# Kernel optimization log

Hardware: AMD Instinct MI355X
Metric: run time of the kernel (lower is better)

## Reference

```python
import jax, jax.numpy as jnp
import numpy as np

TEMPERATURE = 0.07
EPS = 1e-12


def setup_inputs() -> dict:
    key = jax.random.key(0)
    k1, k2 = jax.random.split(key)
    N, D = 8192, 1024
    features = jax.random.normal(k1, (N, D), dtype=jnp.float32)
    labels = jax.random.randint(k2, (N,), 0, 1000, dtype=jnp.int64)
    return {"features": features, "labels": labels}


def reference(features, labels):
    # L2-normalize rows (matches F.normalize(dim=1) with its eps clamp)
    norm = jnp.maximum(jnp.linalg.norm(features, axis=1, keepdims=True), 1e-12)
    f = features / norm
    n = f.shape[0]
    # [N, N] similarity
    sim = jnp.matmul(f, f.T) / TEMPERATURE
    # positive-pair mask from labels
    mask = (labels[:, None] == labels[None, :]).astype(sim.dtype)
    # denominator excludes self-similarity via (1 - eye)
    not_self = 1.0 - jnp.eye(n, dtype=sim.dtype)
    exp_sim = jnp.exp(sim) * not_self
    log_prob = sim - jnp.log(exp_sim.sum(axis=1, keepdims=True) + EPS)
    loss = -(mask * log_prob).sum(axis=1) / (mask.sum(axis=1) + EPS)
    return loss.mean()
```

## Files before the change

kernel.cpp:

```cpp
#include <hip/hip_runtime.h>
#include <hip/hip_bf16.h>

#define N_ROWS 8192
#define DIM 1024
#define TEMP_INV (1.0f / 0.07f)
#define LOG2E 1.4426950408889634f
#define LN2 0.6931471805599453f

typedef __attribute__((ext_vector_type(4))) int i32x4;

__device__ inline void gload_lds16(const void* g, void* l) {
    __builtin_amdgcn_global_load_lds(
        (const __attribute__((address_space(1))) void*)g,
        (__attribute__((address_space(3))) void*)l,
        16, 0, 0);
}

__global__ __launch_bounds__(256) void knorm(const float* __restrict__ X,
                                             char* __restrict__ Q,
                                             float* __restrict__ SC,
                                             float* __restrict__ S1,
                                             float* __restrict__ S2,
                                             float* __restrict__ CNT) {
    const int row = blockIdx.x;
    const int t = threadIdx.x;
    const float* x = X + (size_t)row * DIM;
    float4 v = reinterpret_cast<const float4*>(x)[t];
    float ss = v.x * v.x + v.y * v.y + v.z * v.z + v.w * v.w;
    float mx = fmaxf(fmaxf(fabsf(v.x), fabsf(v.y)), fmaxf(fabsf(v.z), fabsf(v.w)));
    #pragma unroll
    for (int off = 32; off > 0; off >>= 1) {
        ss += __shfl_down(ss, off);
        mx = fmaxf(mx, __shfl_down(mx, off));
    }
    __shared__ float redS[4], redM[4];
    if ((t & 63) == 0) { redS[t >> 6] = ss; redM[t >> 6] = mx; }
    __syncthreads();
    float tot = redS[0] + redS[1] + redS[2] + redS[3];
    float amax = fmaxf(fmaxf(redM[0], redM[1]), fmaxf(redM[2], redM[3]));
    amax = fmaxf(amax, 1e-20f);
    const float norm = fmaxf(sqrtf(tot), 1e-12f);
    const float qmul = 127.0f / amax;
    const float scale = amax / (127.0f * norm);
    int q0 = (int)rintf(v.x * qmul);
    int q1 = (int)rintf(v.y * qmul);
    int q2 = (int)rintf(v.z * qmul);
    int q3 = (int)rintf(v.w * qmul);
    q0 = min(max(q0, -127), 127); q1 = min(max(q1, -127), 127);
    q2 = min(max(q2, -127), 127); q3 = min(max(q3, -127), 127);
    const unsigned packed = (unsigned)(q0 & 0xff) | ((unsigned)(q1 & 0xff) << 8) |
                            ((unsigned)(q2 & 0xff) << 16) | ((unsigned)(q3 & 0xff) << 24);
    reinterpret_cast<unsigned*>(Q + (size_t)row * DIM)[t] = packed;
    if (t == 0) SC[row] = scale;
    if (t == 1) { S1[row] = 0.f; S2[row] = 0.f; CNT[row] = 0.f; }
}

__global__ __launch_bounds__(256) void kgemm(const char* __restrict__ Q,
                                             const float* __restrict__ SC,
                                             const int* __restrict__ labels,
                                             float* __restrict__ S1,
                                             float* __restrict__ S2,
                                             float* __restrict__ CNT) {
    constexpr int BM = 128, BK = 128;
    __shared__ __align__(16) char As[BM * BK];
    __shared__ __align__(16) char Bs[BM * BK];
    __shared__ int labR[BM];
    __shared__ int labC[BM];
    __shared__ float scR[BM];
    __shared__ float scCs[BM];

    const int bid0 = blockIdx.x;
    const int bid = (bid0 & 7) * 260 + (bid0 >> 3);
    int a = (int)((sqrtf(8.0f * (float)bid + 1.0f) - 1.0f) * 0.5f);
    while ((a + 1) * (a + 2) / 2 <= bid) ++a;
    while (a * (a + 1) / 2 > bid) --a;
    const int bx = a;
    const int by = bid - a * (a + 1) / 2;
    const bool diag = (bx == by);
    const int rowBase = by * BM;
    const int colBase = bx * BM;

    const int t = threadIdx.x;
    const int lane = t & 63;
    const int wid = t >> 6;
    const int wr = wid >> 1;
    const int wc = wid & 1;
    const int l16 = lane & 15;
    const int g16 = lane >> 4;

    if (t < 128) { labR[t] = labels[rowBase + t]; scR[t] = SC[rowBase + t]; }
    else {
        labC[t - 128] = labels[colBase + (t - 128)];
        scCs[t - 128] = SC[colBase + (t - 128)] * (TEMP_INV * LOG2E);
    }

    i32x4 acc[4][4];
    #pragma unroll
    for (int m = 0; m < 4; ++m)
        #pragma unroll
        for (int n = 0; n < 4; ++n)
            acc[m][n] = i32x4{0, 0, 0, 0};

    const int srow = t >> 3;
    const int scolL = (t & 7) * 16;
    const int xorb = (l16 & 7) << 4;

    const char* srcA[4];
    const char* srcB[4];
    int dstOff[4];
    #pragma unroll
    for (int i = 0; i < 4; ++i) {
        const int r = i * 32 + srow;
        const int sg = scolL ^ ((r & 7) << 4);
        srcA[i] = Q + (size_t)(rowBase + r) * DIM + sg;
        srcB[i] = Q + (size_t)(colBase + r) * DIM + sg;
        dstOff[i] = r * BK + scolL;
    }

    #pragma unroll
    for (int kt = 0; kt < DIM / BK; ++kt) {
        const int k0 = kt * BK;
        #pragma unroll
        for (int i = 0; i < 4; ++i) {
            gload_lds16(srcA[i] + k0, &As[dstOff[i]]);
            gload_lds16(srcB[i] + k0, &Bs[dstOff[i]]);
        }
        __syncthreads();

        #pragma unroll
        for (int kk = 0; kk < 2; ++kk) {
            const int ck = (kk * 64 + g16 * 16) ^ xorb;
            i32x4 av[4], bv[4];
            #pragma unroll
            for (int m = 0; m < 4; ++m)
                av[m] = *reinterpret_cast<const i32x4*>(&As[(wr * 64 + m * 16 + l16) * BK + ck]);
            #pragma unroll
            for (int n = 0; n < 4; ++n)
                bv[n] = *reinterpret_cast<const i32x4*>(&Bs[(wc * 64 + n * 16 + l16) * BK + ck]);
            #pragma unroll
            for (int m = 0; m < 4; ++m)
                #pragma unroll
                for (int n = 0; n < 4; ++n)
                    acc[m][n] = __builtin_amdgcn_mfma_i32_16x16x64_i8(av[m], bv[n], acc[m][n], 0, 0, 0);
        }
        __syncthreads();
    }

    int labCn[4];
    float scCl2[4];
    #pragma unroll
    for (int n = 0; n < 4; ++n) {
        const int c = wc * 64 + n * 16 + l16;
        labCn[n] = labC[c];
        scCl2[n] = scCs[c];
    }

    const unsigned long long grpmask = 0xFFFFull << (g16 * 16);

    float colE[4]  = {0.f, 0.f, 0.f, 0.f};
    float colS2[4] = {0.f, 0.f, 0.f, 0.f};
    float colC[4]  = {0.f, 0.f, 0.f, 0.f};

    #pragma unroll
    for (int m = 0; m < 4; ++m) {
        const int rloc = wr * 64 + m * 16 + g16 * 4;
        #pragma unroll
        for (int reg = 0; reg < 4; ++reg) {
            const int row = rowBase + rloc + reg;
            const int labRow = labR[rloc + reg];
            const float sRow = scR[rloc + reg];
            float e = 0.f, s2 = 0.f, c = 0.f;
            #pragma unroll
            for (int n = 0; n < 4; ++n) {
                const float arg2 = (float)acc[m][n][reg] * sRow * scCl2[n];
                const int col = colBase + wc * 64 + n * 16 + l16;
                const float ex = __builtin_amdgcn_exp2f(arg2);
                const bool same = (labRow == labCn[n]);
                if (diag) {
                    if (row != col) e += ex;
                } else {
                    e += ex;
                    colE[n] += ex;
                }
                if (same) {
                    const float sim = arg2 * LN2;
                    s2 += sim; c += 1.0f;
                    if (!diag) { colS2[n] += sim; colC[n] += 1.0f; }
                }
            }
            const unsigned long long bal = __ballot(c != 0.f);
            const bool doS = (bal & grpmask) != 0ull;
            #pragma unroll
            for (int off = 1; off < 16; off <<= 1) e += __shfl_xor(e, off);
            if (doS) {
                #pragma unroll
                for (int off = 1; off < 16; off <<= 1) {
                    s2 += __shfl_xor(s2, off);
                    c  += __shfl_xor(c, off);
                }
            }
            if (l16 == 0) {
                atomicAdd(&S1[row], e);
                if (doS) {
                    atomicAdd(&S2[row], s2);
                    atomicAdd(&CNT[row], c);
                }
            }
        }
    }

    if (!diag) {
        #pragma unroll
        for (int n = 0; n < 4; ++n) {
            float ce = colE[n], cs = colS2[n], cc = colC[n];
            const unsigned long long bal = __ballot(cc != 0.f);
            #pragma unroll
            for (int off = 16; off < 64; off <<= 1) ce += __shfl_xor(ce, off);
            if (bal) {
                #pragma unroll
                for (int off = 16; off < 64; off <<= 1) {
                    cs += __shfl_xor(cs, off);
                    cc += __shfl_xor(cc, off);
                }
            }
            if (g16 == 0) {
                const int col = colBase + wc * 64 + n * 16 + l16;
                atomicAdd(&S1[col], ce);
                if (bal) {
                    atomicAdd(&S2[col], cs);
                    atomicAdd(&CNT[col], cc);
                }
            }
        }
    }
}

__global__ __launch_bounds__(1024) void kfinal(const float* __restrict__ S1,
                                               const float* __restrict__ S2,
                                               const float* __restrict__ CNT,
                                               float* __restrict__ out) {
    const int t = threadIdx.x;
    float a = 0.f;
    for (int i = t; i < N_ROWS; i += 1024) {
        const float cnt = CNT[i];
        const float ld = logf(S1[i] + 1e-12f);
        a += (cnt * ld - S2[i]) / (cnt + 1e-12f);
    }
    #pragma unroll
    for (int off = 32; off > 0; off >>= 1) a += __shfl_down(a, off);
    __shared__ float red[16];
    if ((t & 63) == 0) red[t >> 6] = a;
    __syncthreads();
    if (t == 0) {
        float s = 0.f;
        #pragma unroll
        for (int i = 0; i < 16; ++i) s += red[i];
        out[0] = s / (float)N_ROWS;
    }
}

extern "C" void kernel_launch(void* const* d_in, const int* in_sizes, int n_in,
                              void* d_out, int out_size, void* d_ws, size_t ws_size,
                              hipStream_t stream) {
    const float* feat = (const float*)d_in[0];
    const int* labels = (const int*)d_in[1];
    float* out = (float*)d_out;

    char* Q = (char*)d_ws;
    float* SC = (float*)((char*)d_ws + (size_t)N_ROWS * DIM);
    float* S1 = SC + N_ROWS;
    float* S2 = S1 + N_ROWS;
    float* CNT = S2 + N_ROWS;

    constexpr int NT = N_ROWS / 128;
    constexpr int NBLK = NT * (NT + 1) / 2;

    knorm<<<N_ROWS, 256, 0, stream>>>(feat, Q, SC, S1, S2, CNT);
    kgemm<<<NBLK, 256, 0, stream>>>(Q, SC, labels, S1, S2, CNT);
    kfinal<<<1, 1024, 0, stream>>>(S1, S2, CNT, out);
}
```

Measured before the change: 78.05 us.

## Use 8 waves per GEMM block with 64x32 warp tiles

Moves the int8 similarity GEMM from 4 waves (2x2, each with a 64x64 tile) to 8 waves (2x4, each with a 64x32 tile) per 128x128 block. Each thread issues half as many global-to-LDS loads and holds half the accumulators, which cuts register pressure and allows more resident waves to hide memory latency. In exchange, A-fragment LDS reads are duplicated across more waves, there are more epilogue atomics per block, and the MFMA work per wave between barriers is smaller.

```diff
diff --git a/kernel.cpp b/kernel.cpp
--- a/kernel.cpp
+++ b/kernel.cpp
@@ -55,12 +55,12 @@
     if (t == 1) { S1[row] = 0.f; S2[row] = 0.f; CNT[row] = 0.f; }
 }
 
-__global__ __launch_bounds__(256) void kgemm(const char* __restrict__ Q,
-                                             const float* __restrict__ SC,
-                                             const int* __restrict__ labels,
-                                             float* __restrict__ S1,
-                                             float* __restrict__ S2,
-                                             float* __restrict__ CNT) {
+__global__ __launch_bounds__(512, 8) void kgemm(const char* __restrict__ Q,
+                                                const float* __restrict__ SC,
+                                                const int* __restrict__ labels,
+                                                float* __restrict__ S1,
+                                                float* __restrict__ S2,
+                                                float* __restrict__ CNT) {
     constexpr int BM = 128, BK = 128;
     __shared__ __align__(16) char As[BM * BK];
     __shared__ __align__(16) char Bs[BM * BK];
@@ -83,45 +83,48 @@
     const int t = threadIdx.x;
     const int lane = t & 63;
     const int wid = t >> 6;
-    const int wr = wid >> 1;
-    const int wc = wid & 1;
+    const int wr = wid >> 2;
+    const int wc = wid & 3;
     const int l16 = lane & 15;
     const int g16 = lane >> 4;
 
     if (t < 128) { labR[t] = labels[rowBase + t]; scR[t] = SC[rowBase + t]; }
-    else {
+    else if (t < 256) {
         labC[t - 128] = labels[colBase + (t - 128)];
         scCs[t - 128] = SC[colBase + (t - 128)] * (TEMP_INV * LOG2E);
     }
 
-    i32x4 acc[4][4];
+    i32x4 acc[4][2];
     #pragma unroll
     for (int m = 0; m < 4; ++m)
         #pragma unroll
-        for (int n = 0; n < 4; ++n)
+        for (int n = 0; n < 2; ++n)
             acc[m][n] = i32x4{0, 0, 0, 0};
 
     const int srow = t >> 3;
     const int scolL = (t & 7) * 16;
     const int xorb = (l16 & 7) << 4;
 
-    const char* srcA[4];
-    const char* srcB[4];
-    int dstOff[4];
-    #pragma unroll
-    for (int i = 0; i < 4; ++i) {
-        const int r = i * 32 + srow;
+    const char* srcA[2];
+    const char* srcB[2];
+    int dstOff[2];
+    #pragma unroll
+    for (int i = 0; i < 2; ++i) {
+        const int r = i * 64 + srow;
         const int sg = scolL ^ ((r & 7) << 4);
         srcA[i] = Q + (size_t)(rowBase + r) * DIM + sg;
         srcB[i] = Q + (size_t)(colBase + r) * DIM + sg;
         dstOff[i] = r * BK + scolL;
     }
 
+    const int aRowBase = (wr * 64 + l16) * BK;
+    const int bRowBase = (wc * 32 + l16) * BK;
+
     #pragma unroll
     for (int kt = 0; kt < DIM / BK; ++kt) {
         const int k0 = kt * BK;
         #pragma unroll
-        for (int i = 0; i < 4; ++i) {
+        for (int i = 0; i < 2; ++i) {
             gload_lds16(srcA[i] + k0, &As[dstOff[i]]);
             gload_lds16(srcB[i] + k0, &Bs[dstOff[i]]);
         }
@@ -130,36 +133,36 @@
         #pragma unroll
         for (int kk = 0; kk < 2; ++kk) {
             const int ck = (kk * 64 + g16 * 16) ^ xorb;
-            i32x4 av[4], bv[4];
-            #pragma unroll
-            for (int m = 0; m < 4; ++m)
-                av[m] = *reinterpret_cast<const i32x4*>(&As[(wr * 64 + m * 16 + l16) * BK + ck]);
-            #pragma unroll
-            for (int n = 0; n < 4; ++n)
-                bv[n] = *reinterpret_cast<const i32x4*>(&Bs[(wc * 64 + n * 16 + l16) * BK + ck]);
-            #pragma unroll
-            for (int m = 0; m < 4; ++m)
+            i32x4 bv[2];
+            #pragma unroll
+            for (int n = 0; n < 2; ++n)
+                bv[n] = *reinterpret_cast<const i32x4*>(&Bs[bRowBase + n * 16 * BK + ck]);
+            #pragma unroll
+            for (int m = 0; m < 4; ++m) {
+                const i32x4 av = *reinterpret_cast<const i32x4*>(&As[aRowBase + m * 16 * BK + ck]);
                 #pragma unroll
-                for (int n = 0; n < 4; ++n)
-                    acc[m][n] = __builtin_amdgcn_mfma_i32_16x16x64_i8(av[m], bv[n], acc[m][n], 0, 0, 0);
+                for (int n = 0; n < 2; ++n)
+                    acc[m][n] = __builtin_amdgcn_mfma_i32_16x16x64_i8(av, bv[n], acc[m][n], 0, 0, 0);
+            }
         }
         __syncthreads();
     }
 
-    int labCn[4];
-    float scCl2[4];
-    #pragma unroll
-    for (int n = 0; n < 4; ++n) {
-        const int c = wc * 64 + n * 16 + l16;
-        labCn[n] = labC[c];
-        scCl2[n] = scCs[c];
+    int labCn[2];
+    float scCl2[2];
+    int cbase[2];
+    #pragma unroll
+    for (int n = 0; n < 2; ++n) {
+        cbase[n] = wc * 32 + n * 16 + l16;
+        labCn[n] = labC[cbase[n]];
+        scCl2[n] = scCs[cbase[n]];
     }
 
     const unsigned long long grpmask = 0xFFFFull << (g16 * 16);
 
-    float colE[4]  = {0.f, 0.f, 0.f, 0.f};
-    float colS2[4] = {0.f, 0.f, 0.f, 0.f};
-    float colC[4]  = {0.f, 0.f, 0.f, 0.f};
+    float colE[2]  = {0.f, 0.f};
+    float colS2[2] = {0.f, 0.f};
+    float colC[2]  = {0.f, 0.f};
 
     #pragma unroll
     for (int m = 0; m < 4; ++m) {
@@ -171,9 +174,9 @@
             const float sRow = scR[rloc + reg];
             float e = 0.f, s2 = 0.f, c = 0.f;
             #pragma unroll
-            for (int n = 0; n < 4; ++n) {
+            for (int n = 0; n < 2; ++n) {
                 const float arg2 = (float)acc[m][n][reg] * sRow * scCl2[n];
-                const int col = colBase + wc * 64 + n * 16 + l16;
+                const int col = colBase + cbase[n];
                 const float ex = __builtin_amdgcn_exp2f(arg2);
                 const bool same = (labRow == labCn[n]);
                 if (diag) {
@@ -211,7 +214,7 @@
 
     if (!diag) {
         #pragma unroll
-        for (int n = 0; n < 4; ++n) {
+        for (int n = 0; n < 2; ++n) {
             float ce = colE[n], cs = colS2[n], cc = colC[n];
             const unsigned long long bal = __ballot(cc != 0.f);
             #pragma unroll
@@ -224,7 +227,7 @@
                 }
             }
             if (g16 == 0) {
-                const int col = colBase + wc * 64 + n * 16 + l16;
+                const int col = colBase + cbase[n];
                 atomicAdd(&S1[col], ce);
                 if (bal) {
                     atomicAdd(&S2[col], cs);
@@ -276,6 +279,6 @@
     constexpr int NBLK = NT * (NT + 1) / 2;
 
     knorm<<<N_ROWS, 256, 0, stream>>>(feat, Q, SC, S1, S2, CNT);
-    kgemm<<<NBLK, 256, 0, stream>>>(Q, SC, labels, S1, S2, CNT);
+    kgemm<<<NBLK, 512, 0, stream>>>(Q, SC, labels, S1, S2, CNT);
     kfinal<<<1, 1024, 0, stream>>>(S1, S2, CNT, out);
 }
```

Result: slower. 84.95 us (+8.8%).
